# Kernel tuning notes

Hardware: AMD Instinct MI355X
Metric: run time of the kernel (lower is better)

Reference implementation:

```python
import jax, jax.numpy as jnp
import numpy as np

N, E = 50000, 800000
F_IN, F_OUT, H, F_EDGE = 256, 32, 8, 5
LEAKY_SLOPE = 0.2


def setup_inputs() -> dict:
    key = jax.random.key(0)
    ks = jax.random.split(key, 6)
    x = jax.random.normal(ks[0], (N, F_IN), dtype=jnp.float32)
    edge_index = jax.random.randint(ks[1], (2, E), 0, N, dtype=jnp.int64)
    edge_attr = jax.random.normal(ks[2], (E, F_EDGE), dtype=jnp.float32)
    degree_src = jax.random.randint(ks[3], (E,), 0, 64, dtype=jnp.int64)
    # Xavier-uniform params
    lim_W = float(np.sqrt(6.0 / (F_IN + F_OUT)))
    W = jax.random.uniform(ks[4], (H, F_IN, F_OUT), minval=-lim_W, maxval=lim_W, dtype=jnp.float32)
    A = 2 * F_OUT + F_EDGE
    lim_a = float(np.sqrt(6.0 / (H + A)))
    a = jax.random.uniform(ks[5], (H, A), minval=-lim_a, maxval=lim_a, dtype=jnp.float32)
    lim_e = float(np.sqrt(1.0 / F_EDGE))
    W_edge_w = jax.random.uniform(jax.random.fold_in(key, 7), (F_EDGE, F_EDGE), minval=-lim_e, maxval=lim_e, dtype=jnp.float32)
    return {"x": x, "edge_index": edge_index, "edge_attr": edge_attr,
            "degree_src": degree_src, "W": W, "a": a, "W_edge_w": W_edge_w}


def reference(x, edge_index, edge_attr, degree_src, W, a, W_edge_w):
    n = x.shape[0]
    h, f_out = W.shape[0], W.shape[2]
    src, dst = edge_index[0], edge_index[1]
    # per-head projection: (N, H, F_out)
    Wh = jnp.einsum('nf,hfo->nho', x, W)
    # split attention vector instead of materializing the concat
    a_src, a_dst, a_e = a[:, :f_out], a[:, f_out:2 * f_out], a[:, 2 * f_out:]
    ef = edge_attr @ W_edge_w.T                      # (E, F_edge)
    e = (jnp.einsum('eho,ho->eh', Wh[src], a_src)
         + jnp.einsum('eho,ho->eh', Wh[dst], a_dst)
         + ef @ a_e.T)                                # (E, H)
    e = jax.nn.leaky_relu(e, LEAKY_SLOPE)
    scale = 1.0 / jnp.sqrt(jnp.clip(degree_src.astype(jnp.float32), 1.0, None))
    e = e * scale[:, None]
    # segment softmax over src; torch scatter_reduce amax include_self=True with zeros init -> max includes 0
    e_max = jnp.maximum(jax.ops.segment_max(e, src, num_segments=n), 0.0)
    e_exp = jnp.exp(e - e_max[src])
    e_sum = jax.ops.segment_sum(e_exp, src, num_segments=n)
    alpha = e_exp / (e_sum[src] + 1e-16)             # (E, H)
    msg = Wh[dst] * alpha[:, :, None]                # (E, H, F_out)
    out = jax.ops.segment_sum(msg, src, num_segments=n)
    out = jax.nn.elu(out.reshape(n, h * f_out))
    return out, alpha
```

## Files before the change

kernel.cpp:

```cpp
#include <hip/hip_runtime.h>
#include <hip/hip_bf16.h>
#include <math.h>

#define NN 50000
#define NE 800000
#define FIN 256
#define FOUT 32
#define NH 8
#define FE 5
#define AROW 69

typedef float f32x4 __attribute__((ext_vector_type(4)));
typedef short bf16x8 __attribute__((ext_vector_type(8)));

static __device__ __forceinline__ unsigned short f2bf(float f) {
    unsigned u = __float_as_uint(f);
    unsigned r = (u + 0x7FFFu + ((u >> 16) & 1u)) >> 16;
    return (unsigned short)r;
}
static __device__ __forceinline__ float bf2f(unsigned short b) {
    return __uint_as_float(((unsigned)b) << 16);
}

__global__ __launch_bounds__(256) void k_prep(const float* __restrict__ W,
                                              const float* __restrict__ a,
                                              const float* __restrict__ Wew,
                                              float* __restrict__ C,
                                              unsigned short* __restrict__ Bh,
                                              unsigned short* __restrict__ Bl,
                                              unsigned short* __restrict__ Bsh,
                                              unsigned short* __restrict__ Bsl) {
    int t = threadIdx.x;
    if (blockIdx.x == 0) {
        if (t < NH * FE) {
            int h = t / FE, k = t % FE;
            float s = 0.f;
            for (int j = 0; j < FE; ++j) s += a[h * AROW + 2 * FOUT + j] * Wew[j * FE + k];
            C[t] = s;
        }
        int k = t;
        for (int h = 0; h < NH; ++h) {
            float s1v = 0.f, s2v = 0.f;
            for (int o = 0; o < FOUT; ++o) {
                float wv = W[(size_t)h * (FIN * FOUT) + (size_t)k * FOUT + o];
                s1v += wv * a[h * AROW + o];
                s2v += wv * a[h * AROW + FOUT + o];
            }
            unsigned short h1 = f2bf(s1v);
            Bsh[h * 256 + k] = h1;
            Bsl[h * 256 + k] = f2bf(s1v - bf2f(h1));
            unsigned short h2 = f2bf(s2v);
            Bsh[(8 + h) * 256 + k] = h2;
            Bsl[(8 + h) * 256 + k] = f2bf(s2v - bf2f(h2));
        }
    } else {
        int c = blockIdx.x - 1;
        int k = t;
        int h = c >> 5, o = c & 31;
        float f = W[(size_t)h * (FIN * FOUT) + (size_t)k * FOUT + o];
        unsigned short hi = f2bf(f);
        unsigned short lo = f2bf(f - bf2f(hi));
        Bh[c * 256 + k] = hi;
        Bl[c * 256 + k] = lo;
    }
}

__global__ __launch_bounds__(256) void k_gemm_mfma(const float* __restrict__ x,
                                                   const unsigned short* __restrict__ Bh,
                                                   const unsigned short* __restrict__ Bl,
                                                   const unsigned short* __restrict__ Bsh,
                                                   const unsigned short* __restrict__ Bsl,
                                                   unsigned short* __restrict__ Whb,
                                                   float* __restrict__ s1,
                                                   float* __restrict__ s2,
                                                   const int* __restrict__ ei,
                                                   int* __restrict__ counts, int nrows) {
    __shared__ __align__(16) unsigned short Ah[2][64 * 56];
    int t = threadIdx.x;
    int w = t >> 6, l = t & 63;
    int r = l & 15, blk = l >> 4;
    int row0 = blockIdx.x * 64;
    int c0 = w * 64;

    f32x4 acc[4][4];
    f32x4 acc_s = (f32x4)(0.f);
#pragma unroll
    for (int i = 0; i < 4; ++i)
#pragma unroll
        for (int j = 0; j < 4; ++j) acc[i][j] = (f32x4)(0.f);

    int srow = t >> 2, skq = (t & 3) * 8;
    bool arow_ok = (row0 + srow < nrows);
    const float* xp = x + (size_t)(row0 + srow) * FIN + skq;

    f32x4 xa0 = (f32x4)(0.f), xa1 = (f32x4)(0.f);
    if (arow_ok) { xa0 = *(const f32x4*)xp; xa1 = *(const f32x4*)(xp + 4); }

#pragma unroll
    for (int ks = 0; ks < 8; ++ks) {
        const int k0 = ks * 32;
        {
            bf16x8 hi;
            hi[0] = (short)f2bf(xa0.x); hi[1] = (short)f2bf(xa0.y);
            hi[2] = (short)f2bf(xa0.z); hi[3] = (short)f2bf(xa0.w);
            hi[4] = (short)f2bf(xa1.x); hi[5] = (short)f2bf(xa1.y);
            hi[6] = (short)f2bf(xa1.z); hi[7] = (short)f2bf(xa1.w);
            *(bf16x8*)&Ah[ks & 1][srow * 56 + skq] = hi;
        }
        if (ks < 7 && arow_ok) {
            xa0 = *(const f32x4*)(xp + (ks + 1) * 32);
            xa1 = *(const f32x4*)(xp + (ks + 1) * 32 + 4);
        }
        bf16x8 bh[4], bl[4];
#pragma unroll
        for (int ct = 0; ct < 4; ++ct) {
            int c = c0 + ct * 16 + r;
            bh[ct] = *(const bf16x8*)&Bh[c * 256 + k0 + blk * 8];
            bl[ct] = *(const bf16x8*)&Bl[c * 256 + k0 + blk * 8];
        }
        bf16x8 bsh = *(const bf16x8*)&Bsh[r * 256 + k0 + blk * 8];
        bf16x8 bsl = *(const bf16x8*)&Bsl[r * 256 + k0 + blk * 8];
        __syncthreads();
        bf16x8 ah[4];
#pragma unroll
        for (int rt = 0; rt < 4; ++rt)
            ah[rt] = *(const bf16x8*)&Ah[ks & 1][(rt * 16 + r) * 56 + blk * 8];
#pragma unroll
        for (int ct = 0; ct < 4; ++ct) {
#pragma unroll
            for (int rt = 0; rt < 4; ++rt) {
                acc[rt][ct] = __builtin_amdgcn_mfma_f32_16x16x32_bf16(ah[rt], bh[ct], acc[rt][ct], 0, 0, 0);
                acc[rt][ct] = __builtin_amdgcn_mfma_f32_16x16x32_bf16(ah[rt], bl[ct], acc[rt][ct], 0, 0, 0);
            }
        }
        acc_s = __builtin_amdgcn_mfma_f32_16x16x32_bf16(ah[w], bsh, acc_s, 0, 0, 0);
        acc_s = __builtin_amdgcn_mfma_f32_16x16x32_bf16(ah[w], bsl, acc_s, 0, 0, 0);
    }

#pragma unroll
    for (int rt = 0; rt < 4; ++rt) {
#pragma unroll
        for (int reg = 0; reg < 4; ++reg) {
            int row = row0 + rt * 16 + blk * 4 + reg;
            if (row < nrows) {
#pragma unroll
                for (int ct = 0; ct < 4; ++ct)
                    Whb[(size_t)row * 256 + c0 + ct * 16 + r] = f2bf(acc[rt][ct][reg]);
            }
        }
    }
#pragma unroll
    for (int reg = 0; reg < 4; ++reg) {
        int row = row0 + w * 16 + blk * 4 + reg;
        if (row < nrows) {
            if (r < 8) s1[row * NH + r] = acc_s[reg];
            else       s2[row * NH + (r - 8)] = acc_s[reg];
        }
    }
    int e0 = (blockIdx.x * 256 + t) * 4;
    if (e0 + 3 < NE) {
        int4 e4 = *(const int4*)&ei[e0];
        atomicAdd(&counts[e4.x], 1);
        atomicAdd(&counts[e4.y], 1);
        atomicAdd(&counts[e4.z], 1);
        atomicAdd(&counts[e4.w], 1);
    } else {
        for (int q = 0; q < 4; ++q)
            if (e0 + q < NE) atomicAdd(&counts[ei[e0 + q]], 1);
    }
}

__global__ __launch_bounds__(256) void k_scanA(const int* __restrict__ counts,
                                               int* __restrict__ part,
                                               int* __restrict__ bsums, int n) {
    __shared__ int lds[256];
    int t = threadIdx.x;
    int base = blockIdx.x * 1024;
    int i0 = base + t * 4;
    int v0 = (i0 + 0 < n) ? counts[i0 + 0] : 0;
    int v1 = (i0 + 1 < n) ? counts[i0 + 1] : 0;
    int v2 = (i0 + 2 < n) ? counts[i0 + 2] : 0;
    int v3 = (i0 + 3 < n) ? counts[i0 + 3] : 0;
    int l0 = v0, l1 = l0 + v1, l2 = l1 + v2, l3 = l2 + v3;
    lds[t] = l3;
    __syncthreads();
    for (int off = 1; off < 256; off <<= 1) {
        int val = lds[t];
        if (t >= off) val += lds[t - off];
        __syncthreads();
        lds[t] = val;
        __syncthreads();
    }
    int excl = (t == 0) ? 0 : lds[t - 1];
    if (i0 + 0 < n) part[i0 + 0] = excl;
    if (i0 + 1 < n) part[i0 + 1] = excl + l0;
    if (i0 + 2 < n) part[i0 + 2] = excl + l1;
    if (i0 + 3 < n) part[i0 + 3] = excl + l2;
    if (t == 255) bsums[blockIdx.x] = lds[255];
}

__global__ void k_scanB(const int* __restrict__ bsums, int* __restrict__ boffs, int nb) {
    __shared__ int s[64];
    int t = threadIdx.x;
    int v = (t < nb) ? bsums[t] : 0;
    s[t] = v;
    __syncthreads();
    for (int off = 1; off < 64; off <<= 1) {
        int x = s[t];
        if (t >= off) x += s[t - off];
        __syncthreads();
        s[t] = x;
        __syncthreads();
    }
    if (t < nb) boffs[t] = s[t] - v;
}

__global__ __launch_bounds__(256) void k_scanC(int* __restrict__ row_ptr,
                                               const int* __restrict__ boffs, int n, int total) {
    int i = blockIdx.x * 256 + threadIdx.x;
    if (i < n) row_ptr[i] += boffs[i >> 10];
    else if (i == n) row_ptr[n] = total;
}

__global__ __launch_bounds__(256) void k_scatlog(const int* __restrict__ ei,
                                                 const float* __restrict__ eattr,
                                                 const int* __restrict__ degs,
                                                 const float* __restrict__ s1,
                                                 const float* __restrict__ s2,
                                                 const float* __restrict__ C,
                                                 const int* __restrict__ row_ptr,
                                                 int* __restrict__ counts,
                                                 unsigned short* __restrict__ e_perm,
                                                 int2* __restrict__ de_perm) {
    __shared__ float Cl[NH * FE];
    int t = threadIdx.x;
    if (t < NH * FE) Cl[t] = C[t];
    __syncthreads();
    int e = blockIdx.x * 256 + t;
    if (e >= NE) return;
    int src = ei[e], dst = ei[NE + e];
    int dg = degs[e];
    float scale = rsqrtf((float)(dg > 1 ? dg : 1));
    float ea0 = eattr[(size_t)e * FE + 0];
    float ea1 = eattr[(size_t)e * FE + 1];
    float ea2 = eattr[(size_t)e * FE + 2];
    float ea3 = eattr[(size_t)e * FE + 3];
    float ea4 = eattr[(size_t)e * FE + 4];
    float4 s1a = *(const float4*)&s1[src * NH];
    float4 s1b = *(const float4*)&s1[src * NH + 4];
    float4 s2a = *(const float4*)&s2[dst * NH];
    float4 s2b = *(const float4*)&s2[dst * NH + 4];
    float vs1[8] = {s1a.x, s1a.y, s1a.z, s1a.w, s1b.x, s1b.y, s1b.z, s1b.w};
    float vs2[8] = {s2a.x, s2a.y, s2a.z, s2a.w, s2b.x, s2b.y, s2b.z, s2b.w};
    bf16x8 v;
#pragma unroll
    for (int h = 0; h < NH; ++h) {
        float q = vs1[h] + vs2[h] + ea0 * Cl[h * FE + 0] + ea1 * Cl[h * FE + 1] +
                  ea2 * Cl[h * FE + 2] + ea3 * Cl[h * FE + 3] + ea4 * Cl[h * FE + 4];
        q = q > 0.f ? q : 0.2f * q;
        v[h] = (short)f2bf(q * scale);
    }
    int old = atomicSub(&counts[src], 1);
    int p = row_ptr[src] + old - 1;
    *(bf16x8*)&e_perm[(size_t)p * 8] = v;
    de_perm[p] = make_int2(dst, e);
}

__global__ __launch_bounds__(256) void k_smmsg(const int* __restrict__ row_ptr,
                                               const unsigned short* __restrict__ e_perm,
                                               const int2* __restrict__ de_perm,
                                               const unsigned short* __restrict__ Whb,
                                               float* __restrict__ out_alpha,
                                               float* __restrict__ out) {
    __shared__ float al[4][256];
    __shared__ int dl[4][32];
    __shared__ int el[4][32];
    int t = threadIdx.x;
    int w = t >> 6, l = t & 63;
    int n = blockIdx.x * 4 + w;
    if (n >= NN) return;
    int start = row_ptr[n], deg = row_ptr[n + 1] - start;
    int j = l >> 3, h = l & 7;

    float vc[4];
#pragma unroll
    for (int q = 0; q < 4; ++q) {
        int b = j + 8 * q;
        vc[q] = (b < deg) ? bf2f(e_perm[(size_t)(start + b) * 8 + h]) : -1e30f;
    }
    float mx = 0.f;
#pragma unroll
    for (int q = 0; q < 4; ++q) mx = fmaxf(mx, vc[q]);
    for (int b = 32 + j; b < deg; b += 8)
        mx = fmaxf(mx, bf2f(e_perm[(size_t)(start + b) * 8 + h]));
    mx = fmaxf(mx, __shfl_xor(mx, 8));
    mx = fmaxf(mx, __shfl_xor(mx, 16));
    mx = fmaxf(mx, __shfl_xor(mx, 32));
    float m = mx;
    float ex[4];
    float sm = 0.f;
#pragma unroll
    for (int q = 0; q < 4; ++q) { ex[q] = __expf(vc[q] - m); sm += ex[q]; }
    for (int b = 32 + j; b < deg; b += 8)
        sm += __expf(bf2f(e_perm[(size_t)(start + b) * 8 + h]) - m);
    sm += __shfl_xor(sm, 8);
    sm += __shfl_xor(sm, 16);
    sm += __shfl_xor(sm, 32);
    float inv = 1.f / (sm + 1e-16f);
    f32x4 acc = (f32x4)(0.f);
    int hh = l >> 3;
    for (int base = 0; base < deg; base += 32) {
        int cnt = deg - base;
        if (cnt > 32) cnt = 32;
        if (l < cnt) {
            int2 de = de_perm[start + base + l];
            dl[w][l] = de.x;
            el[w][l] = de.y;
        }
        asm volatile("s_waitcnt lgkmcnt(0)" ::: "memory");
#pragma unroll
        for (int q = 0; q < 4; ++q) {
            int b = base + j + 8 * q;
            if (b < deg) {
                float av = (base == 0 ? ex[q]
                                      : __expf(bf2f(e_perm[(size_t)(start + b) * 8 + h]) - m)) * inv;
                al[w][(j + 8 * q) * 8 + h] = av;
                out_alpha[(size_t)el[w][j + 8 * q] * 8 + h] = av;
            }
        }
        asm volatile("s_waitcnt lgkmcnt(0)" ::: "memory");
        for (int jj = 0; jj < cnt; ++jj) {
            int d = dl[w][jj];
            float av = al[w][jj * 8 + hh];
            ushort4 u = *(const ushort4*)&Whb[(size_t)d * 256 + l * 4];
            acc.x += av * bf2f(u.x);
            acc.y += av * bf2f(u.y);
            acc.z += av * bf2f(u.z);
            acc.w += av * bf2f(u.w);
        }
        asm volatile("s_waitcnt lgkmcnt(0)" ::: "memory");
    }
    f32x4 o;
    o.x = acc.x > 0.f ? acc.x : expm1f(acc.x);
    o.y = acc.y > 0.f ? acc.y : expm1f(acc.y);
    o.z = acc.z > 0.f ? acc.z : expm1f(acc.z);
    o.w = acc.w > 0.f ? acc.w : expm1f(acc.w);
    *(f32x4*)&out[(size_t)n * 256 + l * 4] = o;
}

extern "C" void kernel_launch(void* const* d_in, const int* in_sizes, int n_in,
                              void* d_out, int out_size, void* d_ws, size_t ws_size,
                              hipStream_t stream) {
    const float* x     = (const float*)d_in[0];
    const int*   ei    = (const int*)d_in[1];
    const float* eattr = (const float*)d_in[2];
    const int*   degs  = (const int*)d_in[3];
    const float* W     = (const float*)d_in[4];
    const float* a     = (const float*)d_in[5];
    const float* Wew   = (const float*)d_in[6];

    float* out       = (float*)d_out;
    float* out_alpha = out + (size_t)NN * 256;

    char* p = (char*)d_ws;
    auto alloc = [&](size_t bytes) -> char* {
        char* r = p;
        p += (bytes + 255) & ~(size_t)255;
        return r;
    };
    unsigned short* Whb     = (unsigned short*)alloc((size_t)NN * 256 * 2);
    float*          s1      = (float*)alloc((size_t)NN * NH * 4);
    float*          s2      = (float*)alloc((size_t)NN * NH * 4);
    float*          Cm      = (float*)alloc(NH * FE * 4);
    unsigned short* Bh      = (unsigned short*)alloc((size_t)256 * 256 * 2);
    unsigned short* Bl      = (unsigned short*)alloc((size_t)256 * 256 * 2);
    unsigned short* Bsh     = (unsigned short*)alloc((size_t)16 * 256 * 2);
    unsigned short* Bsl     = (unsigned short*)alloc((size_t)16 * 256 * 2);
    int*            counts  = (int*)alloc((size_t)NN * 4);
    int*            row_ptr = (int*)alloc((size_t)(NN + 1) * 4);
    int*            bsums   = (int*)alloc(64 * 4);
    int*            boffs   = (int*)alloc(64 * 4);
    unsigned short* e_perm  = (unsigned short*)alloc((size_t)NE * NH * 2);
    int2*           de_perm = (int2*)alloc((size_t)NE * 8);

    hipMemsetAsync(counts, 0, (size_t)NN * 4, stream);

    k_prep<<<257, 256, 0, stream>>>(W, a, Wew, Cm, Bh, Bl, Bsh, Bsl);
    k_gemm_mfma<<<(NN + 63) / 64, 256, 0, stream>>>(x, Bh, Bl, Bsh, Bsl, Whb, s1, s2,
                                                    ei, counts, NN);
    k_scanA<<<(NN + 1023) / 1024, 256, 0, stream>>>(counts, row_ptr, bsums, NN);
    k_scanB<<<1, 64, 0, stream>>>(bsums, boffs, (NN + 1023) / 1024);
    k_scanC<<<(NN + 1 + 255) / 256, 256, 0, stream>>>(row_ptr, boffs, NN, NE);
    k_scatlog<<<(NE + 255) / 256, 256, 0, stream>>>(ei, eattr, degs, s1, s2, Cm,
                                                    row_ptr, counts, e_perm, de_perm);
    k_smmsg<<<(NN + 3) / 4, 256, 0, stream>>>(row_ptr, e_perm, de_perm, Whb,
                                              out_alpha, out);
}
```

Before: 237.7 us.

## Pre-convert x to bf16 in a separate pass and load GEMM A-operand directly

Adds a kernel that converts x from fp32 to bf16 into a padded workspace buffer and also does the edge-count atomics. The GEMM then reads the A operand straight from global bf16 memory into registers, with no LDS staging and no __syncthreads. This removes the conversion work and the barrier from the GEMM and halves the bytes the GEMM reads for x. In exchange it adds a full write and re-read of a 25.6MB bf16 copy plus an extra launch, and the tail rows read uninitialized padding that is never written back.

```diff
diff --git a/kernel.cpp b/kernel.cpp
--- a/kernel.cpp
+++ b/kernel.cpp
@@ -9,6 +9,7 @@
 #define NH 8
 #define FE 5
 #define AROW 69
+#define NROWS_PAD 50048
 
 typedef float f32x4 __attribute__((ext_vector_type(4)));
 typedef short bf16x8 __attribute__((ext_vector_type(8)));
@@ -65,17 +66,38 @@
     }
 }
 
-__global__ __launch_bounds__(256) void k_gemm_mfma(const float* __restrict__ x,
+__global__ __launch_bounds__(256) void k_pre2(const float* __restrict__ x,
+                                              unsigned short* __restrict__ xb,
+                                              const int* __restrict__ ei,
+                                              int* __restrict__ counts) {
+    int i = blockIdx.x * 256 + threadIdx.x;
+    if (i < (NN * FIN) / 8) {
+        f32x4 u0 = *(const f32x4*)&x[(size_t)i * 8];
+        f32x4 u1 = *(const f32x4*)&x[(size_t)i * 8 + 4];
+        bf16x8 hi;
+        hi[0] = (short)f2bf(u0.x); hi[1] = (short)f2bf(u0.y);
+        hi[2] = (short)f2bf(u0.z); hi[3] = (short)f2bf(u0.w);
+        hi[4] = (short)f2bf(u1.x); hi[5] = (short)f2bf(u1.y);
+        hi[6] = (short)f2bf(u1.z); hi[7] = (short)f2bf(u1.w);
+        *(bf16x8*)&xb[(size_t)i * 8] = hi;
+    }
+    if (i < NE / 4) {
+        int4 e4 = *(const int4*)&ei[i * 4];
+        atomicAdd(&counts[e4.x], 1);
+        atomicAdd(&counts[e4.y], 1);
+        atomicAdd(&counts[e4.z], 1);
+        atomicAdd(&counts[e4.w], 1);
+    }
+}
+
+__global__ __launch_bounds__(256) void k_gemm_mfma(const unsigned short* __restrict__ xb,
                                                    const unsigned short* __restrict__ Bh,
                                                    const unsigned short* __restrict__ Bl,
                                                    const unsigned short* __restrict__ Bsh,
                                                    const unsigned short* __restrict__ Bsl,
                                                    unsigned short* __restrict__ Whb,
                                                    float* __restrict__ s1,
-                                                   float* __restrict__ s2,
-                                                   const int* __restrict__ ei,
-                                                   int* __restrict__ counts, int nrows) {
-    __shared__ __align__(16) unsigned short Ah[2][64 * 56];
+                                                   float* __restrict__ s2, int nrows) {
     int t = threadIdx.x;
     int w = t >> 6, l = t & 63;
     int r = l & 15, blk = l >> 4;
@@ -89,28 +111,18 @@
 #pragma unroll
         for (int j = 0; j < 4; ++j) acc[i][j] = (f32x4)(0.f);
 
-    int srow = t >> 2, skq = (t & 3) * 8;
-    bool arow_ok = (row0 + srow < nrows);
-    const float* xp = x + (size_t)(row0 + srow) * FIN + skq;
-
-    f32x4 xa0 = (f32x4)(0.f), xa1 = (f32x4)(0.f);
-    if (arow_ok) { xa0 = *(const f32x4*)xp; xa1 = *(const f32x4*)(xp + 4); }
+    const unsigned short* ap[4];
+#pragma unroll
+    for (int rt = 0; rt < 4; ++rt)
+        ap[rt] = xb + (size_t)(row0 + rt * 16 + r) * 256 + blk * 8;
 
 #pragma unroll
     for (int ks = 0; ks < 8; ++ks) {
         const int k0 = ks * 32;
-        {
-            bf16x8 hi;
-            hi[0] = (short)f2bf(xa0.x); hi[1] = (short)f2bf(xa0.y);
-            hi[2] = (short)f2bf(xa0.z); hi[3] = (short)f2bf(xa0.w);
-            hi[4] = (short)f2bf(xa1.x); hi[5] = (short)f2bf(xa1.y);
-            hi[6] = (short)f2bf(xa1.z); hi[7] = (short)f2bf(xa1.w);
-            *(bf16x8*)&Ah[ks & 1][srow * 56 + skq] = hi;
-        }
-        if (ks < 7 && arow_ok) {
-            xa0 = *(const f32x4*)(xp + (ks + 1) * 32);
-            xa1 = *(const f32x4*)(xp + (ks + 1) * 32 + 4);
-        }
+        bf16x8 ah[4];
+#pragma unroll
+        for (int rt = 0; rt < 4; ++rt)
+            ah[rt] = *(const bf16x8*)(ap[rt] + k0);
         bf16x8 bh[4], bl[4];
 #pragma unroll
         for (int ct = 0; ct < 4; ++ct) {
@@ -120,11 +132,6 @@
         }
         bf16x8 bsh = *(const bf16x8*)&Bsh[r * 256 + k0 + blk * 8];
         bf16x8 bsl = *(const bf16x8*)&Bsl[r * 256 + k0 + blk * 8];
-        __syncthreads();
-        bf16x8 ah[4];
-#pragma unroll
-        for (int rt = 0; rt < 4; ++rt)
-            ah[rt] = *(const bf16x8*)&Ah[ks & 1][(rt * 16 + r) * 56 + blk * 8];
 #pragma unroll
         for (int ct = 0; ct < 4; ++ct) {
 #pragma unroll
@@ -156,17 +163,6 @@
             if (r < 8) s1[row * NH + r] = acc_s[reg];
             else       s2[row * NH + (r - 8)] = acc_s[reg];
         }
-    }
-    int e0 = (blockIdx.x * 256 + t) * 4;
-    if (e0 + 3 < NE) {
-        int4 e4 = *(const int4*)&ei[e0];
-        atomicAdd(&counts[e4.x], 1);
-        atomicAdd(&counts[e4.y], 1);
-        atomicAdd(&counts[e4.z], 1);
-        atomicAdd(&counts[e4.w], 1);
-    } else {
-        for (int q = 0; q < 4; ++q)
-            if (e0 + q < NE) atomicAdd(&counts[ei[e0 + q]], 1);
     }
 }
 
@@ -369,6 +365,7 @@
         return r;
     };
     unsigned short* Whb     = (unsigned short*)alloc((size_t)NN * 256 * 2);
+    unsigned short* xb      = (unsigned short*)alloc((size_t)NROWS_PAD * 256 * 2);
     float*          s1      = (float*)alloc((size_t)NN * NH * 4);
     float*          s2      = (float*)alloc((size_t)NN * NH * 4);
     float*          Cm      = (float*)alloc(NH * FE * 4);
@@ -386,8 +383,8 @@
     hipMemsetAsync(counts, 0, (size_t)NN * 4, stream);
 
     k_prep<<<257, 256, 0, stream>>>(W, a, Wew, Cm, Bh, Bl, Bsh, Bsl);
-    k_gemm_mfma<<<(NN + 63) / 64, 256, 0, stream>>>(x, Bh, Bl, Bsh, Bsl, Whb, s1, s2,
-                                                    ei, counts, NN);
+    k_pre2<<<(NN * FIN / 8 + 255) / 256, 256, 0, stream>>>(x, xb, ei, counts);
+    k_gemm_mfma<<<(NN + 63) / 64, 256, 0, stream>>>(xb, Bh, Bl, Bsh, Bsl, Whb, s1, s2, NN);
     k_scanA<<<(NN + 1023) / 1024, 256, 0, stream>>>(counts, row_ptr, bsums, NN);
     k_scanB<<<1, 64, 0, stream>>>(bsums, boffs, (NN + 1023) / 1024);
     k_scanC<<<(NN + 1 + 255) / 256, 256, 0, stream>>>(row_ptr, boffs, NN, NE);
```

Measured after the change: 264.6 us. 11.3% more time.
